# Performance work log

Hardware: AMD Instinct MI355X
Metric: run time of the kernel (lower is better)

Reference implementation:

```python
import jax, jax.numpy as jnp
import numpy as np

BN_EPS = 1e-5
NUM_HEADS = 4

def conv1x1_bn_silu(x, w, gamma, beta, mean, var):
    # x: (B,C,H,W), w: (Cout,Cin) -- 1x1 conv, no bias; BN in eval mode; SiLU act
    y = jnp.einsum('bchw,oc->bohw', x, w)
    g = (gamma / jnp.sqrt(var + BN_EPS))[:, None, None]
    b = (beta - mean * gamma / jnp.sqrt(var + BN_EPS))[:, None, None]
    y = y * g + b
    return y * jax.nn.sigmoid(y)

def setup_inputs() -> dict:
    key = jax.random.key(0)
    ks = jax.random.split(key, 16)
    B, H, W, C = 4, 64, 64, 256
    N = H * W
    Ckv = C // 4 * 2  # kv conv out channels = 128
    inp = {
        'x': jax.random.normal(ks[0], (B, N, C), jnp.float32),
        'y': jax.random.normal(ks[1], (B, N, C), jnp.float32),
        'H': H,
        'W': W,
        'q_w': jax.random.normal(ks[2], (C, C), jnp.float32) * (1.0 / np.sqrt(C)),
        'q_gamma': jax.random.uniform(ks[3], (C,), jnp.float32) + 0.5,
        'q_beta': jax.random.normal(ks[4], (C,), jnp.float32) * 0.1,
        'q_mean': jax.random.normal(ks[5], (C,), jnp.float32) * 0.1,
        'q_var': jax.random.uniform(ks[6], (C,), jnp.float32) + 0.5,
        'kv_w': jax.random.normal(ks[7], (Ckv, C), jnp.float32) * (1.0 / np.sqrt(C)),
        'kv_gamma': jax.random.uniform(ks[8], (Ckv,), jnp.float32) + 0.5,
        'kv_beta': jax.random.normal(ks[9], (Ckv,), jnp.float32) * 0.1,
        'kv_mean': jax.random.normal(ks[10], (Ckv,), jnp.float32) * 0.1,
        'kv_var': jax.random.uniform(ks[11], (Ckv,), jnp.float32) + 0.5,
        'proj_w': jax.random.normal(ks[12], (C, C), jnp.float32) * (1.0 / np.sqrt(C)),
        'proj_b': jax.random.normal(ks[13], (C,), jnp.float32) * 0.1,
    }
    return inp

def reference(x, y, H, W, q_w, q_gamma, q_beta, q_mean, q_var,
              kv_w, kv_gamma, kv_beta, kv_mean, kv_var, proj_w, proj_b):
    B, N, C = x.shape
    nh = NUM_HEADS
    hd = C // nh
    scale = hd ** -0.5
    x4 = x.reshape(B, C, H, W)
    y4 = y.reshape(B, C, H, W)
    # q: (B,C,H,W) -> raw reshape (B,N,nh,hd) -> (B,nh,N,hd)  (faithful to torch code)
    q = conv1x1_bn_silu(x4, q_w, q_gamma, q_beta, q_mean, q_var)
    q = q.reshape(B, N, nh, hd).transpose(0, 2, 1, 3)
    # kv: (B,C/2,H,W) -> raw reshape (B,M,2,nh,hd), M = N//4
    kv = conv1x1_bn_silu(y4, kv_w, kv_gamma, kv_beta, kv_mean, kv_var)
    kv = kv.reshape(B, -1, 2, nh, hd).transpose(2, 0, 3, 1, 4)
    k, v = kv[0], kv[1]  # (B,nh,M,hd)
    attn = jnp.einsum('bhnd,bhmd->bhnm', q * scale, k)  # (B,nh,N,M)
    att_map = jax.nn.softmax(attn, axis=-1)
    out = jnp.einsum('bhnm,bhmd->bhnd', att_map, v)  # (B,nh,N,hd)
    out = out.reshape(B, N, C)  # raw reshape, faithful to original
    out = out @ proj_w.T + proj_b
    return out
```

## Files before the change

kernel.cpp:

```cpp
#include <hip/hip_runtime.h>
#include <hip/hip_bf16.h>
#include <math.h>

#define BB 4
#define NTOK 4096
#define CC 256
#define NH 4
#define HD 64
#define CKV 128

typedef _Float16 half8 __attribute__((ext_vector_type(8)));
typedef _Float16 half4 __attribute__((ext_vector_type(4)));
typedef _Float16 half2v __attribute__((ext_vector_type(2)));
typedef float    f32x4 __attribute__((ext_vector_type(4)));
typedef unsigned int uint2v __attribute__((ext_vector_type(2)));

__device__ __forceinline__ half2v pkrtz(float a, float b) {
  return __builtin_bit_cast(half2v, __builtin_amdgcn_cvt_pkrtz(a, b));
}
__device__ __forceinline__ float exp2_fast(float x) {
  float r;
  asm("v_exp_f32 %0, %1" : "=v"(r) : "v"(x));
  return r;
}
__device__ __forceinline__ int swzi(int row, int d) {
  return row * 64 + (d ^ ((row & 7) << 3));
}
__device__ __forceinline__ int swzv(int row, int d) {
  return row * 64 + (d ^ (((row >> 1) & 7) << 3));
}
__device__ __forceinline__ f32x4 mfma16(half8 a, half8 b, f32x4 c) {
  return __builtin_amdgcn_mfma_f32_16x16x32_f16(a, b, c, 0, 0, 0);
}

__global__ __launch_bounds__(256) void pre_all(
    const float* __restrict__ x, const float* __restrict__ y,
    const float* __restrict__ qw, const float* __restrict__ qg_, const float* __restrict__ qb,
    const float* __restrict__ qm, const float* __restrict__ qv,
    const float* __restrict__ kw, const float* __restrict__ kg_, const float* __restrict__ kb,
    const float* __restrict__ km, const float* __restrict__ kvv,
    const float* __restrict__ pw,
    _Float16* __restrict__ Xt, _Float16* __restrict__ Yt,
    _Float16* __restrict__ qWh, float* __restrict__ qB2,
    _Float16* __restrict__ kWh, float* __restrict__ kB2,
    _Float16* __restrict__ pWh)
{
  const int id = blockIdx.x;
  __shared__ float T[64][65];
  const int t = threadIdx.x;
  if (id < 2048) {
    const float* X   = (id < 1024) ? x  : y;
    _Float16*   XT   = (id < 1024) ? Xt : Yt;
    const int i = id & 1023;
    const int pt = i & 63, ct = (i >> 6) & 3, b = i >> 8;
    const float* Xb = X + (size_t)b * CC * NTOK + (size_t)ct * 64 * NTOK + pt * 64;
    const int cr = t >> 4, pc = (t & 15) * 4;
    #pragma unroll
    for (int k = 0; k < 4; ++k) {
      float4 v = *(const float4*)&Xb[(size_t)(cr + k * 16) * NTOK + pc];
      T[cr + k * 16][pc]     = v.x;  T[cr + k * 16][pc + 1] = v.y;
      T[cr + k * 16][pc + 2] = v.z;  T[cr + k * 16][pc + 3] = v.w;
    }
    __syncthreads();
    _Float16* Ot = XT + (size_t)b * NTOK * CC + (size_t)(pt * 64) * CC + ct * 64;
    #pragma unroll
    for (int k = 0; k < 2; ++k) {
      int u = t + k * 256;
      int p = u >> 3, ch = u & 7;
      half8 h;
      #pragma unroll
      for (int j = 0; j < 8; ++j) h[j] = (_Float16)T[ch * 8 + j][p];
      *(half8*)&Ot[(size_t)p * CC + ch * 8] = h;
    }
  } else {
    const int r = id - 2048;
    const int c = t;
    if (r < 256) {
      float g = qg_[r] * rsqrtf(qv[r] + 1e-5f);
      qWh[r * 256 + c] = (_Float16)(qw[r * 256 + c] * g);
      if (c == 0) qB2[r] = qb[r] - qm[r] * g;
    } else if (r < 384) {
      int o = r - 256;
      float g = kg_[o] * rsqrtf(kvv[o] + 1e-5f);
      kWh[o * 256 + c] = (_Float16)(kw[o * 256 + c] * g);
      if (c == 0) kB2[o] = kb[o] - km[o] * g;
    } else if (r < 640) {
      int o = r - 384;
      pWh[o * 256 + c] = (_Float16)pw[o * 256 + c];
    }
  }
}

__global__ __launch_bounds__(256) void conv_mfma_all(
    const _Float16* __restrict__ Xt, const _Float16* __restrict__ Yt,
    const _Float16* __restrict__ qWh, const float* __restrict__ qB2,
    const _Float16* __restrict__ kWh, const float* __restrict__ kB2,
    _Float16* __restrict__ qout, _Float16* __restrict__ kvout)
{
  const int ptile = blockIdx.x, oy = blockIdx.y, b = blockIdx.z;
  const bool isq = oy < 4;
  const _Float16* A  = isq ? Xt : Yt;
  const _Float16* W  = isq ? qWh : kWh;
  const float*    B2 = isq ? qB2 : kB2;
  _Float16*       Y  = isq ? qout : kvout;
  const int otile = isq ? oy : oy - 4;
  const int COUT  = isq ? 256 : 128;

  __shared__ _Float16 Xs[128 * 64];
  __shared__ _Float16 Ws[64 * 64];
  const int t = threadIdx.x, wave = t >> 6, lane = t & 63;
  const int lm = lane & 15, lg = lane >> 4;
  const _Float16* Xb = A + (size_t)b * NTOK * CC + (size_t)ptile * 128 * CC;
  const _Float16* Wb = W + otile * 64 * 256;
  f32x4 acc[2][4];
  #pragma unroll
  for (int m = 0; m < 2; ++m)
    #pragma unroll
    for (int n = 0; n < 4; ++n) acc[m][n] = (f32x4){0.f, 0.f, 0.f, 0.f};

  for (int c0 = 0; c0 < 256; c0 += 64) {
    __syncthreads();
    #pragma unroll
    for (int i = 0; i < 4; ++i) {
      int u = t + i * 256; int p = u >> 3, ch = u & 7;
      *(half8*)&Xs[swzi(p, ch * 8)] = *(const half8*)&Xb[(size_t)p * 256 + c0 + ch * 8];
    }
    #pragma unroll
    for (int i = 0; i < 2; ++i) {
      int u = t + i * 256; int o = u >> 3, ch = u & 7;
      *(half8*)&Ws[swzi(o, ch * 8)] = *(const half8*)&Wb[o * 256 + c0 + ch * 8];
    }
    __syncthreads();
    #pragma unroll
    for (int kh = 0; kh < 2; ++kh) {
      half8 af[2], bf[4];
      #pragma unroll
      for (int m = 0; m < 2; ++m) af[m] = *(half8*)&Xs[swzi(wave * 32 + m * 16 + lm, kh * 32 + lg * 8)];
      #pragma unroll
      for (int n = 0; n < 4; ++n) bf[n] = *(half8*)&Ws[swzi(n * 16 + lm, kh * 32 + lg * 8)];
      #pragma unroll
      for (int m = 0; m < 2; ++m)
        #pragma unroll
        for (int n = 0; n < 4; ++n)
          acc[m][n] = mfma16(af[m], bf[n], acc[m][n]);
    }
  }
  _Float16* Yb = Y + (size_t)b * COUT * NTOK;
  #pragma unroll
  for (int m = 0; m < 2; ++m)
    #pragma unroll
    for (int n = 0; n < 4; ++n) {
      int o = otile * 64 + n * 16 + lm;
      float b2 = B2[o];
      float r[4];
      #pragma unroll
      for (int rr = 0; rr < 4; ++rr) {
        float v = acc[m][n][rr] + b2;
        r[rr] = v / (1.f + __expf(-v));
      }
      half2v p0 = pkrtz(r[0], r[1]);
      half2v p1 = pkrtz(r[2], r[3]);
      half4 h; h[0]=p0[0]; h[1]=p0[1]; h[2]=p1[0]; h[3]=p1[1];
      int p = ptile * 128 + wave * 32 + m * 16 + lg * 4;
      *(half4*)&Yb[(size_t)o * NTOK + p] = h;
    }
}

__global__ __launch_bounds__(256) void attn_mfma6(
    const _Float16* __restrict__ Q,
    const _Float16* __restrict__ KV,
    _Float16* __restrict__ O)
{
  const int nt = blockIdx.x, hh = blockIdx.y, b = blockIdx.z;
  const int n0 = nt * 128;
  const int t = threadIdx.x, wave = t >> 6, lane = t & 63;
  const int lm = lane & 15, lg = lane >> 4;
  const int wq = wave * 32;
  const float SCL = 0.125f * 1.44269504f;

  __shared__ _Float16 Kl[2][64 * 64];
  __shared__ _Float16 Vt[2][64 * 64];
  __shared__ _Float16 Pl[128 * 64];

  const _Float16* Qb  = Q  + (size_t)b * (CC * NTOK)  + hh * 64;
  const _Float16* KVb = KV + (size_t)b * (CKV * NTOK) + hh * 64;

  half8 qf[2][2];
  #pragma unroll
  for (int qg = 0; qg < 2; ++qg) {
    int n = n0 + wq + qg * 16 + lm;
    const _Float16* src = Qb + (n >> 4) * 4096 + (n & 15) * 256;
    qf[qg][0] = *(const half8*)(src + lg * 8);
    qf[qg][1] = *(const half8*)(src + 32 + lg * 8);
  }

  half8 ones;
  #pragma unroll
  for (int j = 0; j < 8; ++j) ones[j] = (_Float16)1.f;

  f32x4 acc[2][4], accl[2];
  float m_run[2];
  #pragma unroll
  for (int qg = 0; qg < 2; ++qg) {
    m_run[qg] = -1e30f;
    accl[qg] = (f32x4){0.f, 0.f, 0.f, 0.f};
    #pragma unroll
    for (int dg = 0; dg < 4; ++dg) acc[qg][dg] = (f32x4){0.f, 0.f, 0.f, 0.f};
  }

  const int kkey = t >> 2, kch = (t & 3) * 2;
  const int dvp = (t & 31) * 2, kgv = t >> 5;
  const _Float16* kp = KVb + (size_t)(kkey >> 3) * 4096 + (kkey & 7) * 512 + kch * 8;
  const _Float16* vp = KVb + (size_t)kgv * 4096 + 256 + dvp;

  half8 kreg[2];
  unsigned int vreg[8];

  auto PREFETCH = [&]() {
    kreg[0] = *(const half8*)kp;
    kreg[1] = *(const half8*)(kp + 8);
    #pragma unroll
    for (int j = 0; j < 8; ++j)
      vreg[j] = *(const unsigned int*)(vp + j * 512);
    kp += 8 * 4096;
    vp += 8 * 4096;
  };
  auto STORE_LDS = [&](int buf) {
    *(half8*)&Kl[buf][swzi(kkey, kch * 8)]       = kreg[0];
    *(half8*)&Kl[buf][swzi(kkey, kch * 8 + 8)]   = kreg[1];
    half8 lo, hi;
    #pragma unroll
    for (int j = 0; j < 8; ++j) {
      half2v hv = __builtin_bit_cast(half2v, vreg[j]);
      lo[j] = hv[0]; hi[j] = hv[1];
    }
    *(half8*)&Vt[buf][swzv(dvp,     kgv * 8)] = lo;
    *(half8*)&Vt[buf][swzv(dvp + 1, kgv * 8)] = hi;
  };

  PREFETCH();
  STORE_LDS(0);
  __syncthreads();

  int cur = 0;
  for (int mt = 0; mt < 16; ++mt) {
    if (mt < 15) PREFETCH();

    f32x4 sc[2][4];
    __builtin_amdgcn_s_setprio(1);
    #pragma unroll
    for (int kt = 0; kt < 4; ++kt) {
      half8 kf0 = *(half8*)&Kl[cur][swzi(kt * 16 + lm, lg * 8)];
      half8 kf1 = *(half8*)&Kl[cur][swzi(kt * 16 + lm, 32 + lg * 8)];
      #pragma unroll
      for (int qg = 0; qg < 2; ++qg) {
        f32x4 z = (f32x4){0.f, 0.f, 0.f, 0.f};
        z = mfma16(kf0, qf[qg][0], z);
        z = mfma16(kf1, qf[qg][1], z);
        sc[qg][kt] = z;
      }
    }
    __builtin_amdgcn_s_setprio(0);

    #pragma unroll
    for (int qg = 0; qg < 2; ++qg) {
      float t0 = fmaxf(fmaxf(sc[qg][0][0], sc[qg][0][1]), sc[qg][0][2]);
      float t1 = fmaxf(fmaxf(sc[qg][0][3], sc[qg][1][0]), sc[qg][1][1]);
      float t2 = fmaxf(fmaxf(sc[qg][1][2], sc[qg][1][3]), sc[qg][2][0]);
      float t3 = fmaxf(fmaxf(sc[qg][2][1], sc[qg][2][2]), sc[qg][2][3]);
      float t4 = fmaxf(fmaxf(sc[qg][3][0], sc[qg][3][1]), sc[qg][3][2]);
      float tm = fmaxf(fmaxf(fmaxf(t0, t1), t2), fmaxf(fmaxf(t3, t4), sc[qg][3][3]));
      tm *= SCL;
      tm = fmaxf(tm, __shfl_xor(tm, 16, 64));
      tm = fmaxf(tm, __shfl_xor(tm, 32, 64));
      if (__any(tm > m_run[qg] + 8.0f)) {
        float mnew = fmaxf(m_run[qg], tm);
        float corr = exp2_fast(m_run[qg] - mnew);
        #pragma unroll
        for (int dg = 0; dg < 4; ++dg) acc[qg][dg] *= corr;
        accl[qg] *= corr;
        m_run[qg] = mnew;
      }
      int qrow = wq + qg * 16 + lm;
      #pragma unroll
      for (int kt = 0; kt < 4; ++kt) {
        float p0 = exp2_fast(fmaf(sc[qg][kt][0], SCL, -m_run[qg]));
        float p1 = exp2_fast(fmaf(sc[qg][kt][1], SCL, -m_run[qg]));
        float p2 = exp2_fast(fmaf(sc[qg][kt][2], SCL, -m_run[qg]));
        float p3 = exp2_fast(fmaf(sc[qg][kt][3], SCL, -m_run[qg]));
        half2v a = pkrtz(p0, p1), c = pkrtz(p2, p3);
        half4 h; h[0]=a[0]; h[1]=a[1]; h[2]=c[0]; h[3]=c[1];
        *(half4*)&Pl[swzi(qrow, kt * 16 + lg * 4)] = h;
      }
    }

    __builtin_amdgcn_s_setprio(1);
    #pragma unroll
    for (int ka = 0; ka < 2; ++ka) {
      half8 pf[2];
      #pragma unroll
      for (int qg = 0; qg < 2; ++qg) {
        pf[qg] = *(half8*)&Pl[swzi(wq + qg * 16 + lm, ka * 32 + lg * 8)];
        accl[qg] = mfma16(ones, pf[qg], accl[qg]);
      }
      #pragma unroll
      for (int dg = 0; dg < 4; ++dg) {
        half8 vf = *(half8*)&Vt[cur][swzv(dg * 16 + lm, ka * 32 + lg * 8)];
        #pragma unroll
        for (int qg = 0; qg < 2; ++qg)
          acc[qg][dg] = mfma16(vf, pf[qg], acc[qg][dg]);
      }
    }
    __builtin_amdgcn_s_setprio(0);

    if (mt < 15) STORE_LDS(cur ^ 1);
    __syncthreads();
    cur ^= 1;
  }

  #pragma unroll
  for (int qg = 0; qg < 2; ++qg) {
    float inv = 1.f / accl[qg][0];
    int n = n0 + wq + qg * 16 + lm;
    _Float16* dst = O + ((size_t)(b * NH + hh) * NTOK + n) * 64;
    #pragma unroll
    for (int dg = 0; dg < 4; ++dg) {
      half2v p0 = pkrtz(acc[qg][dg][0] * inv, acc[qg][dg][1] * inv);
      half2v p1 = pkrtz(acc[qg][dg][2] * inv, acc[qg][dg][3] * inv);
      half4 h; h[0]=p0[0]; h[1]=p0[1]; h[2]=p1[0]; h[3]=p1[1];
      *(half4*)(dst + dg * 16 + lg * 4) = h;
    }
  }
}

__global__ __launch_bounds__(256) void proj_mfma(
    const _Float16* __restrict__ A, const _Float16* __restrict__ Wp,
    const float* __restrict__ bias, float* __restrict__ Out)
{
  const int rtile = blockIdx.x, ctile = blockIdx.y;
  __shared__ _Float16 As[128 * 64];
  __shared__ _Float16 Ws[64 * 64];
  const int t = threadIdx.x, wave = t >> 6, lane = t & 63;
  const int lm = lane & 15, lg = lane >> 4;
  const _Float16* Ab = A + (size_t)rtile * 128 * 256;
  const _Float16* Wb = Wp + ctile * 64 * 256;
  f32x4 acc[2][4];
  #pragma unroll
  for (int m = 0; m < 2; ++m)
    #pragma unroll
    for (int n = 0; n < 4; ++n) acc[m][n] = (f32x4){0.f, 0.f, 0.f, 0.f};

  for (int c0 = 0; c0 < 256; c0 += 64) {
    __syncthreads();
    #pragma unroll
    for (int i = 0; i < 4; ++i) {
      int u = t + i * 256; int r = u >> 3, ch = u & 7;
      *(half8*)&As[swzi(r, ch * 8)] = *(const half8*)&Ab[(size_t)r * 256 + c0 + ch * 8];
    }
    #pragma unroll
    for (int i = 0; i < 2; ++i) {
      int u = t + i * 256; int o = u >> 3, ch = u & 7;
      *(half8*)&Ws[swzi(o, ch * 8)] = *(const half8*)&Wb[o * 256 + c0 + ch * 8];
    }
    __syncthreads();
    #pragma unroll
    for (int kh = 0; kh < 2; ++kh) {
      half8 af[2], bf[4];
      #pragma unroll
      for (int m = 0; m < 2; ++m) af[m] = *(half8*)&As[swzi(wave * 32 + m * 16 + lm, kh * 32 + lg * 8)];
      #pragma unroll
      for (int n = 0; n < 4; ++n) bf[n] = *(half8*)&Ws[swzi(n * 16 + lm, kh * 32 + lg * 8)];
      #pragma unroll
      for (int m = 0; m < 2; ++m)
        #pragma unroll
        for (int n = 0; n < 4; ++n)
          acc[m][n] = mfma16(af[m], bf[n], acc[m][n]);
    }
  }
  float* Ob = Out + (size_t)rtile * 128 * 256 + ctile * 64;
  #pragma unroll
  for (int n = 0; n < 4; ++n) {
    float bia = bias[ctile * 64 + n * 16 + lm];
    #pragma unroll
    for (int m = 0; m < 2; ++m)
      #pragma unroll
      for (int rr = 0; rr < 4; ++rr)
        Ob[(size_t)(wave * 32 + m * 16 + lg * 4 + rr) * 256 + n * 16 + lm] =
            acc[m][n][rr] + bia;
  }
}

extern "C" void kernel_launch(void* const* d_in, const int* in_sizes, int n_in,
                              void* d_out, int out_size, void* d_ws, size_t ws_size,
                              hipStream_t stream) {
  const float* x        = (const float*)d_in[0];
  const float* y        = (const float*)d_in[1];
  const float* q_w      = (const float*)d_in[4];
  const float* q_gamma  = (const float*)d_in[5];
  const float* q_beta   = (const float*)d_in[6];
  const float* q_mean   = (const float*)d_in[7];
  const float* q_var    = (const float*)d_in[8];
  const float* kv_w     = (const float*)d_in[9];
  const float* kv_gamma = (const float*)d_in[10];
  const float* kv_beta  = (const float*)d_in[11];
  const float* kv_mean  = (const float*)d_in[12];
  const float* kv_var   = (const float*)d_in[13];
  const float* proj_w   = (const float*)d_in[14];
  const float* proj_b   = (const float*)d_in[15];
  float* out = (float*)d_out;

  _Float16* Xt   = (_Float16*)d_ws;
  _Float16* Yt   = Xt   + (size_t)BB * NTOK * CC;
  _Float16* qbn  = Yt   + (size_t)BB * NTOK * CC;
  _Float16* kvbn = qbn  + (size_t)BB * CC * NTOK;
  _Float16* aout = kvbn + (size_t)BB * CKV * NTOK;
  _Float16* qWh  = aout + (size_t)BB * NH * NTOK * HD;
  _Float16* kWh  = qWh + 256 * 256;
  _Float16* pWh  = kWh + 128 * 256;
  float* qB2 = (float*)(pWh + 256 * 256);
  float* kB2 = qB2 + 256;

  pre_all<<<2688, 256, 0, stream>>>(
      x, y, q_w, q_gamma, q_beta, q_mean, q_var,
      kv_w, kv_gamma, kv_beta, kv_mean, kv_var, proj_w,
      Xt, Yt, qWh, qB2, kWh, kB2, pWh);
  conv_mfma_all<<<dim3(32, 6, BB), 256, 0, stream>>>(
      Xt, Yt, qWh, qB2, kWh, kB2, qbn, kvbn);
  attn_mfma6<<<dim3(32, NH, BB), 256, 0, stream>>>(qbn, kvbn, aout);
  proj_mfma<<<dim3(128, 4), 256, 0, stream>>>(aout, pWh, proj_b, out);
}
```

Before: 67.07 us.

## Fuse input transpose and BN weight folding into conv MFMA kernel

Removes the separate preprocessing kernel that transposed x/y into fp16 token-major buffers and folded BN into fp16 weights. The conv kernel now reads fp32 inputs directly, transposes them through an LDS staging tile, converts weights to fp16 on the fly, and applies the BN scale and shift in the epilogue. The projection kernel likewise converts fp32 weights inline. This saves one launch and a full write-plus-read of the transposed activations, at the cost of more LDS traffic, an extra barrier per k-step, and redundant weight conversion across blocks (each input tile is re-read by 4 or 2 output tiles).

```diff
diff --git a/kernel.cpp b/kernel.cpp
--- a/kernel.cpp
+++ b/kernel.cpp
@@ -13,7 +13,6 @@
 typedef _Float16 half4 __attribute__((ext_vector_type(4)));
 typedef _Float16 half2v __attribute__((ext_vector_type(2)));
 typedef float    f32x4 __attribute__((ext_vector_type(4)));
-typedef unsigned int uint2v __attribute__((ext_vector_type(2)));
 
 __device__ __forceinline__ half2v pkrtz(float a, float b) {
   return __builtin_bit_cast(half2v, __builtin_amdgcn_cvt_pkrtz(a, b));
@@ -33,85 +32,35 @@
   return __builtin_amdgcn_mfma_f32_16x16x32_f16(a, b, c, 0, 0, 0);
 }
 
-__global__ __launch_bounds__(256) void pre_all(
+__global__ __launch_bounds__(256) void conv_fused(
     const float* __restrict__ x, const float* __restrict__ y,
     const float* __restrict__ qw, const float* __restrict__ qg_, const float* __restrict__ qb,
     const float* __restrict__ qm, const float* __restrict__ qv,
     const float* __restrict__ kw, const float* __restrict__ kg_, const float* __restrict__ kb,
     const float* __restrict__ km, const float* __restrict__ kvv,
-    const float* __restrict__ pw,
-    _Float16* __restrict__ Xt, _Float16* __restrict__ Yt,
-    _Float16* __restrict__ qWh, float* __restrict__ qB2,
-    _Float16* __restrict__ kWh, float* __restrict__ kB2,
-    _Float16* __restrict__ pWh)
-{
-  const int id = blockIdx.x;
-  __shared__ float T[64][65];
-  const int t = threadIdx.x;
-  if (id < 2048) {
-    const float* X   = (id < 1024) ? x  : y;
-    _Float16*   XT   = (id < 1024) ? Xt : Yt;
-    const int i = id & 1023;
-    const int pt = i & 63, ct = (i >> 6) & 3, b = i >> 8;
-    const float* Xb = X + (size_t)b * CC * NTOK + (size_t)ct * 64 * NTOK + pt * 64;
-    const int cr = t >> 4, pc = (t & 15) * 4;
-    #pragma unroll
-    for (int k = 0; k < 4; ++k) {
-      float4 v = *(const float4*)&Xb[(size_t)(cr + k * 16) * NTOK + pc];
-      T[cr + k * 16][pc]     = v.x;  T[cr + k * 16][pc + 1] = v.y;
-      T[cr + k * 16][pc + 2] = v.z;  T[cr + k * 16][pc + 3] = v.w;
-    }
-    __syncthreads();
-    _Float16* Ot = XT + (size_t)b * NTOK * CC + (size_t)(pt * 64) * CC + ct * 64;
-    #pragma unroll
-    for (int k = 0; k < 2; ++k) {
-      int u = t + k * 256;
-      int p = u >> 3, ch = u & 7;
-      half8 h;
-      #pragma unroll
-      for (int j = 0; j < 8; ++j) h[j] = (_Float16)T[ch * 8 + j][p];
-      *(half8*)&Ot[(size_t)p * CC + ch * 8] = h;
-    }
-  } else {
-    const int r = id - 2048;
-    const int c = t;
-    if (r < 256) {
-      float g = qg_[r] * rsqrtf(qv[r] + 1e-5f);
-      qWh[r * 256 + c] = (_Float16)(qw[r * 256 + c] * g);
-      if (c == 0) qB2[r] = qb[r] - qm[r] * g;
-    } else if (r < 384) {
-      int o = r - 256;
-      float g = kg_[o] * rsqrtf(kvv[o] + 1e-5f);
-      kWh[o * 256 + c] = (_Float16)(kw[o * 256 + c] * g);
-      if (c == 0) kB2[o] = kb[o] - km[o] * g;
-    } else if (r < 640) {
-      int o = r - 384;
-      pWh[o * 256 + c] = (_Float16)pw[o * 256 + c];
-    }
-  }
-}
-
-__global__ __launch_bounds__(256) void conv_mfma_all(
-    const _Float16* __restrict__ Xt, const _Float16* __restrict__ Yt,
-    const _Float16* __restrict__ qWh, const float* __restrict__ qB2,
-    const _Float16* __restrict__ kWh, const float* __restrict__ kB2,
     _Float16* __restrict__ qout, _Float16* __restrict__ kvout)
 {
   const int ptile = blockIdx.x, oy = blockIdx.y, b = blockIdx.z;
   const bool isq = oy < 4;
-  const _Float16* A  = isq ? Xt : Yt;
-  const _Float16* W  = isq ? qWh : kWh;
-  const float*    B2 = isq ? qB2 : kB2;
-  _Float16*       Y  = isq ? qout : kvout;
+  const float* Xsrc = isq ? x : y;
+  const float* W    = isq ? qw : kw;
+  const float* gam  = isq ? qg_ : kg_;
+  const float* bet  = isq ? qb : kb;
+  const float* mea  = isq ? qm : km;
+  const float* var  = isq ? qv : kvv;
+  _Float16*    Yout = isq ? qout : kvout;
   const int otile = isq ? oy : oy - 4;
   const int COUT  = isq ? 256 : 128;
 
+  __shared__ float    T[64 * 132];
   __shared__ _Float16 Xs[128 * 64];
   __shared__ _Float16 Ws[64 * 64];
+
   const int t = threadIdx.x, wave = t >> 6, lane = t & 63;
   const int lm = lane & 15, lg = lane >> 4;
-  const _Float16* Xb = A + (size_t)b * NTOK * CC + (size_t)ptile * 128 * CC;
-  const _Float16* Wb = W + otile * 64 * 256;
+  const float* Xb = Xsrc + (size_t)b * CC * NTOK + ptile * 128;
+  const float* Wb = W + otile * 64 * 256;
+
   f32x4 acc[2][4];
   #pragma unroll
   for (int m = 0; m < 2; ++m)
@@ -121,14 +70,32 @@
   for (int c0 = 0; c0 < 256; c0 += 64) {
     __syncthreads();
     #pragma unroll
-    for (int i = 0; i < 4; ++i) {
-      int u = t + i * 256; int p = u >> 3, ch = u & 7;
-      *(half8*)&Xs[swzi(p, ch * 8)] = *(const half8*)&Xb[(size_t)p * 256 + c0 + ch * 8];
+    for (int i = 0; i < 8; ++i) {
+      int c = (t >> 5) + i * 8;
+      int pcol = (t & 31) * 4;
+      *(float4*)&T[c * 132 + pcol] =
+          *(const float4*)&Xb[(size_t)(c0 + c) * NTOK + pcol];
     }
     #pragma unroll
     for (int i = 0; i < 2; ++i) {
       int u = t + i * 256; int o = u >> 3, ch = u & 7;
-      *(half8*)&Ws[swzi(o, ch * 8)] = *(const half8*)&Wb[o * 256 + c0 + ch * 8];
+      const float* ws = &Wb[o * 256 + c0 + ch * 8];
+      half8 h;
+      #pragma unroll
+      for (int j = 0; j < 8; ++j) h[j] = (_Float16)ws[j];
+      *(half8*)&Ws[swzi(o, ch * 8)] = h;
+    }
+    __syncthreads();
+    {
+      int p = t & 127, chh = (t >> 7) * 4;
+      #pragma unroll
+      for (int cc = 0; cc < 4; ++cc) {
+        int ch = chh + cc;
+        half8 h;
+        #pragma unroll
+        for (int j = 0; j < 8; ++j) h[j] = (_Float16)T[(ch * 8 + j) * 132 + p];
+        *(half8*)&Xs[swzi(p, ch * 8)] = h;
+      }
     }
     __syncthreads();
     #pragma unroll
@@ -145,17 +112,25 @@
           acc[m][n] = mfma16(af[m], bf[n], acc[m][n]);
     }
   }
-  _Float16* Yb = Y + (size_t)b * COUT * NTOK;
+
+  float ga[4], bb[4];
+  #pragma unroll
+  for (int n = 0; n < 4; ++n) {
+    int o = otile * 64 + n * 16 + lm;
+    float g = gam[o] * rsqrtf(var[o] + 1e-5f);
+    ga[n] = g;
+    bb[n] = bet[o] - mea[o] * g;
+  }
+  _Float16* Yb = Yout + (size_t)b * COUT * NTOK;
   #pragma unroll
   for (int m = 0; m < 2; ++m)
     #pragma unroll
     for (int n = 0; n < 4; ++n) {
       int o = otile * 64 + n * 16 + lm;
-      float b2 = B2[o];
       float r[4];
       #pragma unroll
       for (int rr = 0; rr < 4; ++rr) {
-        float v = acc[m][n][rr] + b2;
+        float v = acc[m][n][rr] * ga[n] + bb[n];
         r[rr] = v / (1.f + __expf(-v));
       }
       half2v p0 = pkrtz(r[0], r[1]);
@@ -334,7 +309,7 @@
 }
 
 __global__ __launch_bounds__(256) void proj_mfma(
-    const _Float16* __restrict__ A, const _Float16* __restrict__ Wp,
+    const _Float16* __restrict__ A, const float* __restrict__ Wp,
     const float* __restrict__ bias, float* __restrict__ Out)
 {
   const int rtile = blockIdx.x, ctile = blockIdx.y;
@@ -343,7 +318,7 @@
   const int t = threadIdx.x, wave = t >> 6, lane = t & 63;
   const int lm = lane & 15, lg = lane >> 4;
   const _Float16* Ab = A + (size_t)rtile * 128 * 256;
-  const _Float16* Wb = Wp + ctile * 64 * 256;
+  const float* Wb = Wp + ctile * 64 * 256;
   f32x4 acc[2][4];
   #pragma unroll
   for (int m = 0; m < 2; ++m)
@@ -360,7 +335,11 @@
     #pragma unroll
     for (int i = 0; i < 2; ++i) {
       int u = t + i * 256; int o = u >> 3, ch = u & 7;
-      *(half8*)&Ws[swzi(o, ch * 8)] = *(const half8*)&Wb[o * 256 + c0 + ch * 8];
+      const float* ws = &Wb[o * 256 + c0 + ch * 8];
+      half8 h;
+      #pragma unroll
+      for (int j = 0; j < 8; ++j) h[j] = (_Float16)ws[j];
+      *(half8*)&Ws[swzi(o, ch * 8)] = h;
     }
     __syncthreads();
     #pragma unroll
@@ -409,23 +388,13 @@
   const float* proj_b   = (const float*)d_in[15];
   float* out = (float*)d_out;
 
-  _Float16* Xt   = (_Float16*)d_ws;
-  _Float16* Yt   = Xt   + (size_t)BB * NTOK * CC;
-  _Float16* qbn  = Yt   + (size_t)BB * NTOK * CC;
+  _Float16* qbn  = (_Float16*)d_ws;
   _Float16* kvbn = qbn  + (size_t)BB * CC * NTOK;
   _Float16* aout = kvbn + (size_t)BB * CKV * NTOK;
-  _Float16* qWh  = aout + (size_t)BB * NH * NTOK * HD;
-  _Float16* kWh  = qWh + 256 * 256;
-  _Float16* pWh  = kWh + 128 * 256;
-  float* qB2 = (float*)(pWh + 256 * 256);
-  float* kB2 = qB2 + 256;
-
-  pre_all<<<2688, 256, 0, stream>>>(
+
+  conv_fused<<<dim3(32, 6, BB), 256, 0, stream>>>(
       x, y, q_w, q_gamma, q_beta, q_mean, q_var,
-      kv_w, kv_gamma, kv_beta, kv_mean, kv_var, proj_w,
-      Xt, Yt, qWh, qB2, kWh, kB2, pWh);
-  conv_mfma_all<<<dim3(32, 6, BB), 256, 0, stream>>>(
-      Xt, Yt, qWh, qB2, kWh, kB2, qbn, kvbn);
+      kv_w, kv_gamma, kv_beta, kv_mean, kv_var, qbn, kvbn);
   attn_mfma6<<<dim3(32, NH, BB), 256, 0, stream>>>(qbn, kvbn, aout);
-  proj_mfma<<<dim3(128, 4), 256, 0, stream>>>(aout, pWh, proj_b, out);
-}
+  proj_mfma<<<dim3(128, 4), 256, 0, stream>>>(aout, proj_w, proj_b, out);
+}
```

After: 63.16 us. -5.8%, faster.
